# Performance work log

Hardware: AMD Instinct MI355X
Metric: run time of the kernel (lower is better)

Reference implementation:

```python
import jax, jax.numpy as jnp
import numpy as np

B, N, D, H = 1, 2048, 2048, 16
K = D // H  # head dim = 128


def setup_inputs() -> dict:
    key = jax.random.key(0)
    k1, k2, k3 = jax.random.split(key, 3)
    x = jax.random.normal(k1, (B, N, D), dtype=jnp.float32)
    # torch Linear(D, 3D, bias=False): y = x @ W.T; we store the transposed weight directly.
    W_qkv = jax.random.normal(k2, (D, 3 * D), dtype=jnp.float32) * 0.02
    W_out = jax.random.normal(k3, (D, D), dtype=jnp.float32) * 0.02
    return {"x": x, "W_qkv": W_qkv, "W_out": W_out}


def reference(x, W_qkv, W_out):
    b, n, d = x.shape
    qkv = (x @ W_qkv).reshape(b, n, 3, H, K)  # [B,N,3,H,K]
    q, k, v = qkv[:, :, 0], qkv[:, :, 1], qkv[:, :, 2]  # each [B,N,H,K]
    scale = np.float32(1.0 / np.sqrt(K))
    scores = jnp.einsum('bnhk,bmhk->bnhm', q, k) * scale  # [B,N,H,M]
    causal_mask = jnp.tril(jnp.ones((n, n), dtype=bool))  # [N,M]
    scores = jnp.where(causal_mask[None, :, None, :], scores, jnp.float32(-jnp.inf))
    probs = jax.nn.softmax(scores, axis=-1)
    attn = jnp.einsum('bnhm,bmhk->bnhk', probs, v).reshape(b, n, d)
    return attn @ W_out
```

## Files before the change

### kernel.cpp

```cpp
#include <hip/hip_runtime.h>
#include <hip/hip_bf16.h>
#include <math.h>

#define N_SEQ  2048
#define DMODEL 2048
#define NHEAD  16
#define HDIM   128
#define QKV_LD 6144

typedef __attribute__((ext_vector_type(8))) short bf16x8;
typedef __attribute__((ext_vector_type(4))) float f32x4;

__device__ __forceinline__ ushort f2bf(float x) {
    union { float f; unsigned u; } v; v.f = x;
    unsigned r = (v.u + 0x7fffu + ((v.u >> 16) & 1u)) >> 16;
    return (ushort)r;
}
__device__ __forceinline__ float bf2f(ushort h) {
    union { unsigned u; float f; } v; v.u = ((unsigned)h) << 16;
    return v.f;
}

__global__ __launch_bounds__(256)
void convert_split(const float* __restrict__ in, ushort* __restrict__ oh,
                   ushort* __restrict__ ol, int n4)
{
    int i = blockIdx.x * 256 + threadIdx.x;
    if (i >= n4) return;
    float4 v = ((const float4*)in)[i];
    ushort4 h, l;
    h.x = f2bf(v.x); l.x = f2bf(v.x - bf2f(h.x));
    h.y = f2bf(v.y); l.y = f2bf(v.y - bf2f(h.y));
    h.z = f2bf(v.z); l.z = f2bf(v.z - bf2f(h.z));
    h.w = f2bf(v.w); l.w = f2bf(v.w - bf2f(h.w));
    ((ushort4*)oh)[i] = h;
    ((ushort4*)ol)[i] = l;
}

__global__ __launch_bounds__(256)
void convert_split_t(const float* __restrict__ in, ushort* __restrict__ oh,
                     ushort* __restrict__ ol, int R, int C)
{
    __shared__ float T[64][65];
    const int t = threadIdx.x;
    const int c0 = blockIdx.x * 64, r0 = blockIdx.y * 64;
    #pragma unroll
    for (int p = 0; p < 4; ++p) {
        int r = (t >> 4) + p * 16;
        int c4 = (t & 15) * 4;
        float4 v = *(const float4*)&in[(size_t)(r0 + r) * C + c0 + c4];
        T[r][c4] = v.x; T[r][c4 + 1] = v.y; T[r][c4 + 2] = v.z; T[r][c4 + 3] = v.w;
    }
    __syncthreads();
    #pragma unroll
    for (int p = 0; p < 4; ++p) {
        int c = (t >> 4) + p * 16;
        int r4 = (t & 15) * 4;
        float f0 = T[r4][c], f1 = T[r4 + 1][c], f2 = T[r4 + 2][c], f3 = T[r4 + 3][c];
        ushort4 h, l;
        h.x = f2bf(f0); l.x = f2bf(f0 - bf2f(h.x));
        h.y = f2bf(f1); l.y = f2bf(f1 - bf2f(h.y));
        h.z = f2bf(f2); l.z = f2bf(f2 - bf2f(h.z));
        h.w = f2bf(f3); l.w = f2bf(f3 - bf2f(h.w));
        *(ushort4*)&oh[(size_t)(c0 + c) * R + r0 + r4] = h;
        *(ushort4*)&ol[(size_t)(c0 + c) * R + r0 + r4] = l;
    }
}

__global__ __launch_bounds__(256)
void transpose_v(const ushort* __restrict__ qkvh, ushort* __restrict__ vt)
{
    __shared__ ushort T[64][72];
    const int t = threadIdx.x;
    const int c0 = blockIdx.x * 64, n0 = blockIdx.y * 64;
    #pragma unroll
    for (int p = 0; p < 2; ++p) {
        int r = (t >> 3) + p * 32;
        int u = (t & 7) * 8;
        *(bf16x8*)&T[r][u] = *(const bf16x8*)&qkvh[(size_t)(n0 + r) * QKV_LD + 2 * DMODEL + c0 + u];
    }
    __syncthreads();
    #pragma unroll
    for (int p = 0; p < 2; ++p) {
        int d = (t >> 3) + p * 32;
        int ju = (t & 7) * 8;
        bf16x8 o;
        #pragma unroll
        for (int i = 0; i < 8; ++i) o[i] = (short)T[ju + i][d];
        *(bf16x8*)&vt[(size_t)(c0 + d) * N_SEQ + n0 + ju] = o;
    }
}

template<bool BF16OUT>
__global__ __launch_bounds__(256, 2)
void gemm_bf16x3_v3(const ushort* __restrict__ Ah_g, const ushort* __restrict__ Al_g,
                    const ushort* __restrict__ Bh_g, const ushort* __restrict__ Bl_g,
                    ushort* __restrict__ Ch, ushort* __restrict__ Cl,
                    float* __restrict__ Cf, int M, int N, int K)
{
    __shared__ ushort bufA[2][128 * 68];
    __shared__ ushort bufB[2][128 * 68];

    const int t = threadIdx.x;
    const int l = t & 63, w = t >> 6;
    const int l15 = l & 15, kgr = l >> 4;
    const int wm = (w >> 1) * 64, wn = (w & 1) * 64;

    const int nbx = N / 128;
    const int nwg = nbx * (M / 128);
    int flat = blockIdx.x + blockIdx.y * nbx;
    if ((nwg & 7) == 0) flat = (flat & 7) * (nwg >> 3) + (flat >> 3);
    const int bm = (flat / nbx) * 128;
    const int bn = (flat % nbx) * 128;

    const int rA = t >> 1;
    const int hA = t & 1;
    const ushort* gA = (hA ? Al_g : Ah_g) + (size_t)(bm + rA) * K;
    const ushort* gB = (hA ? Bl_g : Bh_g) + (size_t)(bn + rA) * K;

    bf16x8 stA[4], stB[4];
    auto load_regs = [&](int k0) {
        #pragma unroll
        for (int j = 0; j < 4; ++j) {
            stA[j] = *(const bf16x8*)(gA + k0 + j * 8);
            stB[j] = *(const bf16x8*)(gB + k0 + j * 8);
        }
    };
    auto write_lds = [&](int bsel) {
        #pragma unroll
        for (int j = 0; j < 4; ++j) {
            *(bf16x8*)&bufA[bsel][rA * 68 + hA * 32 + j * 8] = stA[j];
            *(bf16x8*)&bufB[bsel][rA * 68 + hA * 32 + j * 8] = stB[j];
        }
    };

    f32x4 acc[4][4] = {};
    const int nt = K / 32;
    load_regs(0);
    write_lds(0);
    load_regs(32);

    for (int i = 0; i < nt; ++i) {
        const int c = i & 1;
        asm volatile("s_waitcnt lgkmcnt(0)\n\ts_barrier" ::: "memory");
        if (i + 1 < nt) write_lds(c ^ 1);
        if (i + 2 < nt) load_regs((i + 2) * 32);

        bf16x8 bh[4], bl[4];
        #pragma unroll
        for (int nf = 0; nf < 4; ++nf) {
            const int r = wn + nf * 16 + l15;
            bh[nf] = *(const bf16x8*)&bufB[c][r * 68 + kgr * 8];
            bl[nf] = *(const bf16x8*)&bufB[c][r * 68 + 32 + kgr * 8];
        }
        #pragma unroll
        for (int mf = 0; mf < 4; ++mf) {
            const int r = wm + mf * 16 + l15;
            bf16x8 ah = *(const bf16x8*)&bufA[c][r * 68 + kgr * 8];
            bf16x8 al = *(const bf16x8*)&bufA[c][r * 68 + 32 + kgr * 8];
            #pragma unroll
            for (int nf = 0; nf < 4; ++nf) {
                acc[mf][nf] = __builtin_amdgcn_mfma_f32_16x16x32_bf16(ah, bh[nf], acc[mf][nf], 0, 0, 0);
                acc[mf][nf] = __builtin_amdgcn_mfma_f32_16x16x32_bf16(ah, bl[nf], acc[mf][nf], 0, 0, 0);
                acc[mf][nf] = __builtin_amdgcn_mfma_f32_16x16x32_bf16(al, bh[nf], acc[mf][nf], 0, 0, 0);
            }
        }
    }

    #pragma unroll
    for (int mf = 0; mf < 4; ++mf)
        #pragma unroll
        for (int nf = 0; nf < 4; ++nf)
            #pragma unroll
            for (int r = 0; r < 4; ++r) {
                const int m = bm + wm + mf * 16 + kgr * 4 + r;
                const int n = bn + wn + nf * 16 + l15;
                const float v = acc[mf][nf][r];
                if constexpr (BF16OUT) {
                    ushort h = f2bf(v);
                    Ch[(size_t)m * N + n] = h;
                    Cl[(size_t)m * N + n] = f2bf(v - bf2f(h));
                } else {
                    Cf[(size_t)m * N + n] = v;
                }
            }
}

__global__ __launch_bounds__(256)
void attn_mfma2(const ushort* __restrict__ qkvh, const ushort* __restrict__ qkvl,
                const ushort* __restrict__ vt,
                ushort* __restrict__ oh, ushort* __restrict__ ol)
{
    __shared__ ushort Kh[2][64 * 136], Kl[2][64 * 136];
    __shared__ ushort Vts[2][128 * 68];
    __shared__ ushort St[4][32 * 68];

    const int t = threadIdx.x;
    const int l = t & 63;
    const int w = t >> 6;
    const int l15 = l & 15, kgr = l >> 4;
    const int h = blockIdx.y, b = blockIdx.x;
    const int q00 = b * 64 + w * 16;
    const int q01 = (31 - b) * 64 + w * 16;
    const int ntiles = 32 - b;

    bf16x8 qh[2][4], ql[2][4];
    #pragma unroll
    for (int f = 0; f < 2; ++f) {
        const size_t base = (size_t)((f ? q01 : q00) + l15) * QKV_LD + h * HDIM;
        #pragma unroll
        for (int kc = 0; kc < 4; ++kc) {
            qh[f][kc] = *(const bf16x8*)(qkvh + base + kc * 32 + kgr * 8);
            ql[f][kc] = *(const bf16x8*)(qkvl + base + kc * 32 + kgr * 8);
        }
    }

    f32x4 o[2][8] = {};
    float m_run[2][4], l_run[2][4];
    #pragma unroll
    for (int f = 0; f < 2; ++f)
        #pragma unroll
        for (int r = 0; r < 4; ++r) { m_run[f][r] = -1e30f; l_run[f][r] = 0.f; }

    bf16x8 sKh[4], sKl[4], sV[4];
    auto load_tile = [&](int jb) {
        #pragma unroll
        for (int i = 0; i < 4; ++i) {
            int r = (t >> 4) + i * 16;
            size_t g = (size_t)(jb + r) * QKV_LD + DMODEL + h * HDIM + (t & 15) * 8;
            sKh[i] = *(const bf16x8*)(qkvh + g);
            sKl[i] = *(const bf16x8*)(qkvl + g);
        }
        #pragma unroll
        for (int i = 0; i < 4; ++i) {
            int d = (t >> 3) + i * 32;
            sV[i] = *(const bf16x8*)(vt + (size_t)(h * HDIM + d) * N_SEQ + jb + (t & 7) * 8);
        }
    };
    auto write_tile = [&](int c) {
        #pragma unroll
        for (int i = 0; i < 4; ++i) {
            int r = (t >> 4) + i * 16;
            *(bf16x8*)&Kh[c][r * 136 + (t & 15) * 8] = sKh[i];
            *(bf16x8*)&Kl[c][r * 136 + (t & 15) * 8] = sKl[i];
        }
        #pragma unroll
        for (int i = 0; i < 4; ++i) {
            int d = (t >> 3) + i * 32;
            *(bf16x8*)&Vts[c][d * 68 + (t & 7) * 8] = sV[i];
        }
    };

    const float scale = 0.08838834764831845f;

    load_tile(0);
    write_tile(0);
    load_tile(64);

    for (int jt = 0; jt < ntiles; ++jt) {
        const int jb = jt * 64;
        const int c = jt & 1;
        asm volatile("s_waitcnt lgkmcnt(0)\n\ts_barrier" ::: "memory");
        if (jt + 1 < ntiles) write_tile(c ^ 1);
        if (jt + 2 < ntiles) load_tile(jb + 128);

        const bool f0on = (jt <= b);

        float sv[2][4][4];
        #pragma unroll
        for (int jf = 0; jf < 4; ++jf) {
            f32x4 sacc0 = {}, sacc1 = {};
            #pragma unroll
            for (int kc = 0; kc < 4; ++kc) {
                bf16x8 kh = *(const bf16x8*)&Kh[c][(jf * 16 + l15) * 136 + kc * 32 + kgr * 8];
                bf16x8 kl = *(const bf16x8*)&Kl[c][(jf * 16 + l15) * 136 + kc * 32 + kgr * 8];
                sacc1 = __builtin_amdgcn_mfma_f32_16x16x32_bf16(qh[1][kc], kh, sacc1, 0, 0, 0);
                sacc1 = __builtin_amdgcn_mfma_f32_16x16x32_bf16(qh[1][kc], kl, sacc1, 0, 0, 0);
                sacc1 = __builtin_amdgcn_mfma_f32_16x16x32_bf16(ql[1][kc], kh, sacc1, 0, 0, 0);
                if (f0on) {
                    sacc0 = __builtin_amdgcn_mfma_f32_16x16x32_bf16(qh[0][kc], kh, sacc0, 0, 0, 0);
                    sacc0 = __builtin_amdgcn_mfma_f32_16x16x32_bf16(qh[0][kc], kl, sacc0, 0, 0, 0);
                    sacc0 = __builtin_amdgcn_mfma_f32_16x16x32_bf16(ql[0][kc], kh, sacc0, 0, 0, 0);
                }
            }
            const int j = jb + jf * 16 + l15;
            #pragma unroll
            for (int r = 0; r < 4; ++r) {
                sv[1][jf][r] = (j > q01 + kgr * 4 + r) ? -1e30f : sacc1[r] * scale;
                if (f0on)
                    sv[0][jf][r] = (j > q00 + kgr * 4 + r) ? -1e30f : sacc0[r] * scale;
            }
        }

        float corr[2][4];
        #pragma unroll
        for (int f = 0; f < 2; ++f) {
            if (f == 0 && !f0on) continue;
            #pragma unroll
            for (int r = 0; r < 4; ++r) {
                float tm = fmaxf(fmaxf(sv[f][0][r], sv[f][1][r]),
                                 fmaxf(sv[f][2][r], sv[f][3][r]));
                tm = fmaxf(tm, __shfl_xor(tm, 1));
                tm = fmaxf(tm, __shfl_xor(tm, 2));
                tm = fmaxf(tm, __shfl_xor(tm, 4));
                tm = fmaxf(tm, __shfl_xor(tm, 8));
                const float nm = fmaxf(m_run[f][r], tm);
                corr[f][r] = __expf(m_run[f][r] - nm);
                m_run[f][r] = nm;
                float rs = 0.f;
                const int row = f * 16 + kgr * 4 + r;
                #pragma unroll
                for (int jf = 0; jf < 4; ++jf) {
                    const float pv = __expf(sv[f][jf][r] - nm);
                    St[w][row * 68 + jf * 16 + l15] = f2bf(pv);
                    rs += pv;
                }
                rs += __shfl_xor(rs, 1);
                rs += __shfl_xor(rs, 2);
                rs += __shfl_xor(rs, 4);
                rs += __shfl_xor(rs, 8);
                l_run[f][r] = l_run[f][r] * corr[f][r] + rs;
            }
        }

        #pragma unroll
        for (int f = 0; f < 2; ++f) {
            if (f == 0 && !f0on) continue;
            #pragma unroll
            for (int df = 0; df < 8; ++df)
                #pragma unroll
                for (int r = 0; r < 4; ++r) o[f][df][r] *= corr[f][r];
        }

        #pragma unroll
        for (int jc = 0; jc < 2; ++jc) {
            bf16x8 pa1 = *(const bf16x8*)&St[w][(16 + l15) * 68 + jc * 32 + kgr * 8];
            bf16x8 pa0 = {};
            if (f0on) pa0 = *(const bf16x8*)&St[w][l15 * 68 + jc * 32 + kgr * 8];
            #pragma unroll
            for (int df = 0; df < 8; ++df) {
                bf16x8 vb = *(const bf16x8*)&Vts[c][(df * 16 + l15) * 68 + jc * 32 + kgr * 8];
                o[1][df] = __builtin_amdgcn_mfma_f32_16x16x32_bf16(pa1, vb, o[1][df], 0, 0, 0);
                if (f0on)
                    o[0][df] = __builtin_amdgcn_mfma_f32_16x16x32_bf16(pa0, vb, o[0][df], 0, 0, 0);
            }
        }
    }

    #pragma unroll
    for (int f = 0; f < 2; ++f)
        #pragma unroll
        for (int r = 0; r < 4; ++r) l_run[f][r] = 1.f / l_run[f][r];
    #pragma unroll
    for (int f = 0; f < 2; ++f) {
        const int q0 = f ? q01 : q00;
        #pragma unroll
        for (int df = 0; df < 8; ++df)
            #pragma unroll
            for (int r = 0; r < 4; ++r) {
                const float v = o[f][df][r] * l_run[f][r];
                const size_t a = (size_t)(q0 + kgr * 4 + r) * DMODEL + h * HDIM + df * 16 + l15;
                const ushort hh = f2bf(v);
                oh[a] = hh;
                ol[a] = f2bf(v - bf2f(hh));
            }
    }
}

extern "C" void kernel_launch(void* const* d_in, const int* in_sizes, int n_in,
                              void* d_out, int out_size, void* d_ws, size_t ws_size,
                              hipStream_t stream)
{
    const float* x    = (const float*)d_in[0];
    const float* Wqkv = (const float*)d_in[1];
    const float* Wout = (const float*)d_in[2];
    float* outp = (float*)d_out;

    const size_t O_XHI = 0;
    const size_t O_XLO = 8388608;
    const size_t O_WT  = 16777216;
    const size_t O_QKV = 67108864;

    char* ws = (char*)d_ws;
    ushort* x_hi   = (ushort*)(ws + O_XHI);
    ushort* x_lo   = (ushort*)(ws + O_XLO);
    ushort* wqt_hi = (ushort*)(ws + O_WT);
    ushort* wqt_lo = (ushort*)(ws + O_WT + 25165824);
    ushort* qkv_hi = (ushort*)(ws + O_QKV);
    ushort* qkv_lo = (ushort*)(ws + O_QKV + 25165824);
    ushort* wot_hi = (ushort*)(ws + O_WT);
    ushort* wot_lo = (ushort*)(ws + O_WT + 8388608);
    ushort* vt     = (ushort*)(ws + O_WT + 16777216);
    ushort* at_hi  = (ushort*)(ws + O_XHI);
    ushort* at_lo  = (ushort*)(ws + O_XLO);

    convert_split<<<dim3(N_SEQ * DMODEL / 4 / 256), 256, 0, stream>>>(
        x, x_hi, x_lo, N_SEQ * DMODEL / 4);
    convert_split_t<<<dim3(QKV_LD / 64, DMODEL / 64), 256, 0, stream>>>(
        Wqkv, wqt_hi, wqt_lo, DMODEL, QKV_LD);
    gemm_bf16x3_v3<true><<<dim3(QKV_LD / 128, N_SEQ / 128), 256, 0, stream>>>(
        x_hi, x_lo, wqt_hi, wqt_lo, qkv_hi, qkv_lo, nullptr,
        N_SEQ, QKV_LD, DMODEL);
    convert_split_t<<<dim3(DMODEL / 64, DMODEL / 64), 256, 0, stream>>>(
        Wout, wot_hi, wot_lo, DMODEL, DMODEL);
    transpose_v<<<dim3(DMODEL / 64, N_SEQ / 64), 256, 0, stream>>>(qkv_hi, vt);
    attn_mfma2<<<dim3(16, NHEAD), 256, 0, stream>>>(
        qkv_hi, qkv_lo, vt, at_hi, at_lo);
    gemm_bf16x3_v3<false><<<dim3(DMODEL / 128, N_SEQ / 128), 256, 0, stream>>>(
        at_hi, at_lo, wot_hi, wot_lo, nullptr, nullptr, outp,
        N_SEQ, DMODEL, DMODEL);
}
```

Before: 561.2 us.

## Deepen GEMM global-load prefetch and use smaller tiles for output projection

```diff
diff --git a/kernel.cpp b/kernel.cpp
--- a/kernel.cpp
+++ b/kernel.cpp
@@ -91,86 +91,89 @@
     }
 }
 
-template<bool BF16OUT>
+template<int BM, int BN, bool BF16OUT>
 __global__ __launch_bounds__(256, 2)
-void gemm_bf16x3_v3(const ushort* __restrict__ Ah_g, const ushort* __restrict__ Al_g,
-                    const ushort* __restrict__ Bh_g, const ushort* __restrict__ Bl_g,
-                    ushort* __restrict__ Ch, ushort* __restrict__ Cl,
-                    float* __restrict__ Cf, int M, int N, int K)
-{
-    __shared__ ushort bufA[2][128 * 68];
-    __shared__ ushort bufB[2][128 * 68];
+void gemm_v4(const ushort* __restrict__ Ah_g, const ushort* __restrict__ Al_g,
+             const ushort* __restrict__ Bh_g, const ushort* __restrict__ Bl_g,
+             ushort* __restrict__ Ch, ushort* __restrict__ Cl,
+             float* __restrict__ Cf, int M, int N, int K)
+{
+    constexpr int GA = BM / 64, GB = BN / 64;
+    constexpr int MF = BM / 32, NF = BN / 32;
+    __shared__ ushort bufA[2][BM * 68];
+    __shared__ ushort bufB[2][BN * 68];
 
     const int t = threadIdx.x;
-    const int l = t & 63, w = t >> 6;
-    const int l15 = l & 15, kgr = l >> 4;
-    const int wm = (w >> 1) * 64, wn = (w & 1) * 64;
-
-    const int nbx = N / 128;
-    const int nwg = nbx * (M / 128);
-    int flat = blockIdx.x + blockIdx.y * nbx;
-    if ((nwg & 7) == 0) flat = (flat & 7) * (nwg >> 3) + (flat >> 3);
-    const int bm = (flat / nbx) * 128;
-    const int bn = (flat % nbx) * 128;
-
-    const int rA = t >> 1;
-    const int hA = t & 1;
-    const ushort* gA = (hA ? Al_g : Ah_g) + (size_t)(bm + rA) * K;
-    const ushort* gB = (hA ? Bl_g : Bh_g) + (size_t)(bn + rA) * K;
-
-    bf16x8 stA[4], stB[4];
-    auto load_regs = [&](int k0) {
-        #pragma unroll
-        for (int j = 0; j < 4; ++j) {
-            stA[j] = *(const bf16x8*)(gA + k0 + j * 8);
-            stB[j] = *(const bf16x8*)(gB + k0 + j * 8);
-        }
-    };
-    auto write_lds = [&](int bsel) {
-        #pragma unroll
-        for (int j = 0; j < 4; ++j) {
-            *(bf16x8*)&bufA[bsel][rA * 68 + hA * 32 + j * 8] = stA[j];
-            *(bf16x8*)&bufB[bsel][rA * 68 + hA * 32 + j * 8] = stB[j];
-        }
-    };
-
-    f32x4 acc[4][4] = {};
+    const int l15 = t & 15, kgr = (t >> 4) & 3;
+    const int w = t >> 6;
+    const int wm = (w >> 1) * (BM / 2), wn = (w & 1) * (BN / 2);
+    const int bm = blockIdx.y * BM, bn = blockIdx.x * BN;
+    const int sr = t >> 2, sku = (t & 3) * 8;
+
+    const ushort* pAh = Ah_g + (size_t)(bm + sr) * K + sku;
+    const ushort* pAl = Al_g + (size_t)(bm + sr) * K + sku;
+    const ushort* pBh = Bh_g + (size_t)(bn + sr) * K + sku;
+    const ushort* pBl = Bl_g + (size_t)(bn + sr) * K + sku;
+
+    bf16x8 sA0[2 * GA], sB0[2 * GB], sA1[2 * GA], sB1[2 * GB];
+    f32x4 acc[MF][NF] = {};
     const int nt = K / 32;
-    load_regs(0);
-    write_lds(0);
-    load_regs(32);
-
-    for (int i = 0; i < nt; ++i) {
-        const int c = i & 1;
-        asm volatile("s_waitcnt lgkmcnt(0)\n\ts_barrier" ::: "memory");
-        if (i + 1 < nt) write_lds(c ^ 1);
-        if (i + 2 < nt) load_regs((i + 2) * 32);
-
-        bf16x8 bh[4], bl[4];
-        #pragma unroll
-        for (int nf = 0; nf < 4; ++nf) {
-            const int r = wn + nf * 16 + l15;
-            bh[nf] = *(const bf16x8*)&bufB[c][r * 68 + kgr * 8];
-            bl[nf] = *(const bf16x8*)&bufB[c][r * 68 + 32 + kgr * 8];
-        }
-        #pragma unroll
-        for (int mf = 0; mf < 4; ++mf) {
-            const int r = wm + mf * 16 + l15;
-            bf16x8 ah = *(const bf16x8*)&bufA[c][r * 68 + kgr * 8];
-            bf16x8 al = *(const bf16x8*)&bufA[c][r * 68 + 32 + kgr * 8];
-            #pragma unroll
-            for (int nf = 0; nf < 4; ++nf) {
-                acc[mf][nf] = __builtin_amdgcn_mfma_f32_16x16x32_bf16(ah, bh[nf], acc[mf][nf], 0, 0, 0);
-                acc[mf][nf] = __builtin_amdgcn_mfma_f32_16x16x32_bf16(ah, bl[nf], acc[mf][nf], 0, 0, 0);
-                acc[mf][nf] = __builtin_amdgcn_mfma_f32_16x16x32_bf16(al, bh[nf], acc[mf][nf], 0, 0, 0);
-            }
-        }
-    }
-
-    #pragma unroll
-    for (int mf = 0; mf < 4; ++mf)
-        #pragma unroll
-        for (int nf = 0; nf < 4; ++nf)
+
+#define G_LOAD(SA, SB, k0) do { \
+    _Pragma("unroll") for (int g = 0; g < GA; ++g) { \
+        SA[2*g]   = *(const bf16x8*)(pAh + (size_t)(64*g) * K + (k0)); \
+        SA[2*g+1] = *(const bf16x8*)(pAl + (size_t)(64*g) * K + (k0)); } \
+    _Pragma("unroll") for (int g = 0; g < GB; ++g) { \
+        SB[2*g]   = *(const bf16x8*)(pBh + (size_t)(64*g) * K + (k0)); \
+        SB[2*g+1] = *(const bf16x8*)(pBl + (size_t)(64*g) * K + (k0)); } \
+} while (0)
+
+#define L_WRITE(SA, SB, c) do { \
+    _Pragma("unroll") for (int g = 0; g < GA; ++g) { \
+        *(bf16x8*)&bufA[c][(sr + 64*g) * 68 + sku]      = SA[2*g]; \
+        *(bf16x8*)&bufA[c][(sr + 64*g) * 68 + 32 + sku] = SA[2*g+1]; } \
+    _Pragma("unroll") for (int g = 0; g < GB; ++g) { \
+        *(bf16x8*)&bufB[c][(sr + 64*g) * 68 + sku]      = SB[2*g]; \
+        *(bf16x8*)&bufB[c][(sr + 64*g) * 68 + 32 + sku] = SB[2*g+1]; } \
+} while (0)
+
+#define K_STEP(I, SA, SB, c) do { \
+    asm volatile("s_waitcnt lgkmcnt(0)\n\ts_barrier" ::: "memory"); \
+    if ((I) + 1 < nt) L_WRITE(SA, SB, (c) ^ 1); \
+    if ((I) + 3 < nt) G_LOAD(SA, SB, ((I) + 3) * 32); \
+    bf16x8 bh[NF], bl[NF]; \
+    _Pragma("unroll") for (int nf = 0; nf < NF; ++nf) { \
+        const int r = wn + nf * 16 + l15; \
+        bh[nf] = *(const bf16x8*)&bufB[c][r * 68 + kgr * 8]; \
+        bl[nf] = *(const bf16x8*)&bufB[c][r * 68 + 32 + kgr * 8]; } \
+    _Pragma("unroll") for (int mf = 0; mf < MF; ++mf) { \
+        const int r = wm + mf * 16 + l15; \
+        bf16x8 ah = *(const bf16x8*)&bufA[c][r * 68 + kgr * 8]; \
+        bf16x8 al = *(const bf16x8*)&bufA[c][r * 68 + 32 + kgr * 8]; \
+        _Pragma("unroll") for (int nf = 0; nf < NF; ++nf) { \
+            acc[mf][nf] = __builtin_amdgcn_mfma_f32_16x16x32_bf16(ah, bh[nf], acc[mf][nf], 0, 0, 0); \
+            acc[mf][nf] = __builtin_amdgcn_mfma_f32_16x16x32_bf16(ah, bl[nf], acc[mf][nf], 0, 0, 0); \
+            acc[mf][nf] = __builtin_amdgcn_mfma_f32_16x16x32_bf16(al, bh[nf], acc[mf][nf], 0, 0, 0); } } \
+} while (0)
+
+    G_LOAD(sA0, sB0, 0);
+    L_WRITE(sA0, sB0, 0);
+    G_LOAD(sA1, sB1, 32);
+    G_LOAD(sA0, sB0, 64);
+
+    for (int i = 0; i < nt; i += 2) {
+        K_STEP(i,     sA1, sB1, 0);
+        K_STEP(i + 1, sA0, sB0, 1);
+    }
+
+#undef G_LOAD
+#undef L_WRITE
+#undef K_STEP
+
+    #pragma unroll
+    for (int mf = 0; mf < MF; ++mf)
+        #pragma unroll
+        for (int nf = 0; nf < NF; ++nf)
             #pragma unroll
             for (int r = 0; r < 4; ++r) {
                 const int m = bm + wm + mf * 16 + kgr * 4 + r;
@@ -398,7 +401,7 @@
         x, x_hi, x_lo, N_SEQ * DMODEL / 4);
     convert_split_t<<<dim3(QKV_LD / 64, DMODEL / 64), 256, 0, stream>>>(
         Wqkv, wqt_hi, wqt_lo, DMODEL, QKV_LD);
-    gemm_bf16x3_v3<true><<<dim3(QKV_LD / 128, N_SEQ / 128), 256, 0, stream>>>(
+    gemm_v4<128, 128, true><<<dim3(QKV_LD / 128, N_SEQ / 128), 256, 0, stream>>>(
         x_hi, x_lo, wqt_hi, wqt_lo, qkv_hi, qkv_lo, nullptr,
         N_SEQ, QKV_LD, DMODEL);
     convert_split_t<<<dim3(DMODEL / 64, DMODEL / 64), 256, 0, stream>>>(
@@ -406,7 +409,7 @@
     transpose_v<<<dim3(DMODEL / 64, N_SEQ / 64), 256, 0, stream>>>(qkv_hi, vt);
     attn_mfma2<<<dim3(16, NHEAD), 256, 0, stream>>>(
         qkv_hi, qkv_lo, vt, at_hi, at_lo);
-    gemm_bf16x3_v3<false><<<dim3(DMODEL / 128, N_SEQ / 128), 256, 0, stream>>>(
+    gemm_v4<64, 128, false><<<dim3(DMODEL / 128, N_SEQ / 64), 256, 0, stream>>>(
         at_hi, at_lo, wot_hi, wot_lo, nullptr, nullptr, outp,
         N_SEQ, DMODEL, DMODEL);
 }
```

After: 488.9 us. 1.15x faster.
